# Optimization experiments

Hardware: AMD Instinct MI355X
Metric: run time of the kernel (lower is better)

## Reference

```python
import jax, jax.numpy as jnp
import numpy as np

LATENT, HID, STYLE, D, B = 16, 512, 64, 8, 16384


def _lin(key, fan_in, fan_out):
    kw, kb = jax.random.split(key)
    s = 1.0 / np.sqrt(fan_in)
    return (jax.random.uniform(kw, (fan_in, fan_out), jnp.float32, -s, s),
            jax.random.uniform(kb, (fan_out,), jnp.float32, -s, s))


def setup_inputs() -> dict:
    key = jax.random.key(0)
    ks = jax.random.split(key, 12)
    x = jax.random.normal(ks[0], (B, LATENT), jnp.float32)
    y = jax.random.randint(ks[1], (B,), 0, D)
    # shared MLP: latent->512, 512->512 x3, each followed by ReLU
    W0, b0 = _lin(ks[2], LATENT, HID)
    W1, b1 = _lin(ks[3], HID, HID)
    W2, b2 = _lin(ks[4], HID, HID)
    W3, b3 = _lin(ks[5], HID, HID)
    # unshared per-domain 4-layer MLPs, stacked along domain axis d
    def _stack(k, fi, fo):
        Ws, bs = [], []
        for kk in jax.random.split(k, D):
            w, b = _lin(kk, fi, fo)
            Ws.append(w); bs.append(b)
        return jnp.stack(Ws), jnp.stack(bs)
    U0, c0 = _stack(ks[6], HID, HID)
    U1, c1 = _stack(ks[7], HID, HID)
    U2, c2 = _stack(ks[8], HID, HID)
    U3, c3 = _stack(ks[9], HID, STYLE)
    return {"x": x, "y": y,
            "W0": W0, "b0": b0, "W1": W1, "b1": b1,
            "W2": W2, "b2": b2, "W3": W3, "b3": b3,
            "U0": U0, "c0": c0, "U1": U1, "c1": c1,
            "U2": U2, "c2": c2, "U3": U3, "c3": c3}


def reference(x, y, W0, b0, W1, b1, W2, b2, W3, b3,
              U0, c0, U1, c1, U2, c2, U3, c3):
    # shared trunk
    h = jax.nn.relu(x @ W0 + b0)
    h = jax.nn.relu(h @ W1 + b1)
    h = jax.nn.relu(h @ W2 + b2)
    h = jax.nn.relu(h @ W3 + b3)            # [B, HID]
    # run all D expert MLPs batched, then select per-sample by domain y
    g = jax.nn.relu(jnp.einsum('bi,dio->dbo', h, U0) + c0[:, None, :])
    g = jax.nn.relu(jnp.einsum('dbi,dio->dbo', g, U1) + c1[:, None, :])
    g = jax.nn.relu(jnp.einsum('dbi,dio->dbo', g, U2) + c2[:, None, :])
    g = jnp.einsum('dbi,dio->dbo', g, U3) + c3[:, None, :]   # [D, B, STYLE]
    out = g[y, jnp.arange(g.shape[1])]       # [B, STYLE]
    return out
```

## Files before the change

### kernel.cpp

```cpp
#include <hip/hip_runtime.h>

typedef _Float16 f16;
typedef _Float16 f16x4 __attribute__((ext_vector_type(4)));
typedef _Float16 f16x8 __attribute__((ext_vector_type(8)));
typedef float f32x4 __attribute__((ext_vector_type(4)));

#define B_TOT 16384
#define LAT_  16
#define STY_  64
#define ND_   8

#define ROWS 64
#define NTHR 1024
#define NBLK 256

#define RSTR 40
#define SLAB (64 * RSTR)
#define ACT_LDS (16 * SLAB)

__global__ void prep_k(const float* W0, f16* Wt0, const float* W1, f16* Wt1,
                       const float* W2, f16* Wt2, const float* W3, f16* Wt3,
                       const float* U0, f16* U0t, const float* U1, f16* U1t,
                       const float* U2, f16* U2t, const float* U3, f16* U3t) {
  int z = blockIdx.z;
  const float* src; f16* dst; int Kin, Nin, Kpad, NR;
  if (z == 0)      { src = W0; dst = Wt0; Kin = 16;  Nin = 512; Kpad = 32;  NR = 512; }
  else if (z == 1) { src = W1; dst = Wt1; Kin = 512; Nin = 512; Kpad = 512; NR = 512; }
  else if (z == 2) { src = W2; dst = Wt2; Kin = 512; Nin = 512; Kpad = 512; NR = 512; }
  else if (z == 3) { src = W3; dst = Wt3; Kin = 512; Nin = 512; Kpad = 512; NR = 512; }
  else if (z < 12) { int d = z - 4;  src = U0 + (long)d * 262144; dst = U0t + (long)d * 262144; Kin = 512; Nin = 512; Kpad = 512; NR = 512; }
  else if (z < 20) { int d = z - 12; src = U1 + (long)d * 262144; dst = U1t + (long)d * 262144; Kin = 512; Nin = 512; Kpad = 512; NR = 512; }
  else if (z < 28) { int d = z - 20; src = U2 + (long)d * 262144; dst = U2t + (long)d * 262144; Kin = 512; Nin = 512; Kpad = 512; NR = 512; }
  else             { int d = z - 28; src = U3 + (long)d * 32768;  dst = U3t + (long)d * 32768;  Kin = 512; Nin = 64;  Kpad = 512; NR = 64; }

  __shared__ float tile[32][33];
  int k0 = blockIdx.y * 32, n0 = blockIdx.x * 32;
  int tx = threadIdx.x, ty = threadIdx.y;
  #pragma unroll
  for (int i = 0; i < 32; i += 8) {
    int k = k0 + ty + i, n = n0 + tx;
    tile[ty + i][tx] = (k < Kin && n < Nin) ? src[(long)k * Nin + n] : 0.f;
  }
  __syncthreads();
  #pragma unroll
  for (int i = 0; i < 32; i += 8) {
    int n = n0 + ty + i, k = k0 + tx;
    if (n < NR && k < Kpad)
      dst[(long)(((k >> 5) * NR + n) << 5) | (k & 31)] = (f16)tile[tx][ty + i];
  }
}

#define NT_BUCKET 1024
#define RPT 16

__global__ __launch_bounds__(NT_BUCKET) void bucket_k(const int* __restrict__ y,
                                                      int* __restrict__ offsets,
                                                      int* __restrict__ perm) {
  __shared__ int hist[ND_][NT_BUCKET];
  __shared__ int totals[ND_];
  __shared__ int bases[ND_ + 1];
  int t = threadIdx.x;
  int base = t * RPT;

  #pragma unroll
  for (int d = 0; d < ND_; d++) hist[d][t] = 0;
  int yv[RPT];
  #pragma unroll
  for (int i = 0; i < RPT; i++) {
    yv[i] = y[base + i];
    hist[yv[i]][t]++;
  }
  __syncthreads();

  int wave = t >> 6, lane = t & 63;
  if (wave < ND_) {
    int d = wave;
    int carry = 0;
    for (int c = 0; c < NT_BUCKET; c += 64) {
      int v = hist[d][c + lane];
      int s = v;
      #pragma unroll
      for (int off = 1; off < 64; off <<= 1) {
        int u = __shfl_up(s, off, 64);
        if (lane >= off) s += u;
      }
      hist[d][c + lane] = carry + s - v;
      carry += __shfl(s, 63, 64);
    }
    if (lane == 0) totals[d] = carry;
  }
  __syncthreads();

  if (t == 0) {
    int s = 0;
    #pragma unroll
    for (int d = 0; d < ND_; d++) { bases[d] = s; offsets[d] = s; s += totals[d]; }
    bases[ND_] = s; offsets[ND_] = s;
  }
  __syncthreads();

  #pragma unroll
  for (int i = 0; i < RPT; i++) {
    int d = yv[i];
    int pos = bases[d] + hist[d][t];
    hist[d][t]++;
    perm[pos] = base + i;
  }
}

#define MFMA_(b, a, c) __builtin_amdgcn_mfma_f32_16x16x32_f16((b), (a), (c), 0, 0, 0)

template<int KT, bool FINAL>
__device__ __forceinline__ void do_layer(
    const f16* __restrict__ Wk, const float* __restrict__ bias,
    f16* __restrict__ act, int rlo, int rhi,
    const int* __restrict__ perm, int slot0, float* __restrict__ out, int t) {
  const int lane = t & 63, wid = t >> 6;
  const int lr = lane & 15, lg = lane >> 4;
  char* actb = (char*)act;

  __syncthreads();

  if (!FINAL) {
    const int wn = wid * 32;
    const f16* wp0 = Wk + ((wn + lr) * 32 + lg * 8);
    const f16* wp1 = Wk + ((wn + 16 + lr) * 32 + lg * 8);
    const char* ab[4];
    #pragma unroll
    for (int m = 0; m < 4; m++)
      ab[m] = actb + (m * 16 + lr) * 80 + lg * 16;

    f32x4 acc[4][2];
    #pragma unroll
    for (int m = 0; m < 4; m++) {
      acc[m][0] = f32x4{0.f, 0.f, 0.f, 0.f};
      acc[m][1] = f32x4{0.f, 0.f, 0.f, 0.f};
    }

    f16x8 a0[4], a1[4], b00, b01, b10, b11;
    b00 = *(const f16x8*)wp0;
    b01 = *(const f16x8*)wp1;
    #pragma unroll
    for (int m = 0; m < 4; m++) a0[m] = *(const f16x8*)(ab[m]);

    if constexpr (KT == 1) {
      #pragma unroll
      for (int m = 0; m < 4; m++) {
        acc[m][0] = MFMA_(b00, a0[m], acc[m][0]);
        acc[m][1] = MFMA_(b01, a0[m], acc[m][1]);
      }
    } else {
      #pragma unroll
      for (int kt2 = 0; kt2 < KT / 2; kt2++) {
        const int k1 = 2 * kt2 + 1, k2 = 2 * kt2 + 2;
        b10 = *(const f16x8*)(wp0 + k1 * 16384);
        b11 = *(const f16x8*)(wp1 + k1 * 16384);
        #pragma unroll
        for (int m = 0; m < 4; m++) a1[m] = *(const f16x8*)(ab[m] + k1 * 5120);
        #pragma unroll
        for (int m = 0; m < 4; m++) {
          acc[m][0] = MFMA_(b00, a0[m], acc[m][0]);
          acc[m][1] = MFMA_(b01, a0[m], acc[m][1]);
        }
        if (kt2 < KT / 2 - 1) {
          b00 = *(const f16x8*)(wp0 + k2 * 16384);
          b01 = *(const f16x8*)(wp1 + k2 * 16384);
          #pragma unroll
          for (int m = 0; m < 4; m++) a0[m] = *(const f16x8*)(ab[m] + k2 * 5120);
        }
        #pragma unroll
        for (int m = 0; m < 4; m++) {
          acc[m][0] = MFMA_(b10, a1[m], acc[m][0]);
          acc[m][1] = MFMA_(b11, a1[m], acc[m][1]);
        }
      }
    }

    __syncthreads();

    #pragma unroll
    for (int m = 0; m < 4; m++) {
      int r = m * 16 + lr;
      bool ok = (r >= rlo) && (r < rhi);
      #pragma unroll
      for (int n = 0; n < 2; n++) {
        int cl = n * 16 + lg * 4;
        f32x4 bb = *(const f32x4*)(bias + wn + cl);
        f16x4 h;
        #pragma unroll
        for (int j = 0; j < 4; j++)
          h[j] = (f16)fmaxf(acc[m][n][j] + bb[j], 0.f);
        if (ok)
          *(f16x4*)(actb + wid * 5120 + r * 80 + cl * 2) = h;
      }
    }
  } else {
    const int mf = wid >> 2, nf = wid & 3;
    const f16* wp = Wk + ((nf * 16 + lr) * 32 + lg * 8);
    const char* abf = actb + (mf * 16 + lr) * 80 + lg * 16;
    f32x4 a = f32x4{0.f, 0.f, 0.f, 0.f};
    #pragma unroll
    for (int kt = 0; kt < 16; kt++) {
      f16x8 bf = *(const f16x8*)(wp + kt * 2048);
      f16x8 af = *(const f16x8*)(abf + kt * 5120);
      a = MFMA_(bf, af, a);
    }
    int r = mf * 16 + lr;
    if (r >= rlo && r < rhi) {
      int orig = perm[slot0 + r];
      int cn0 = nf * 16 + lg * 4;
      f32x4 bb = *(const f32x4*)(bias + cn0);
      f32x4 v;
      #pragma unroll
      for (int j = 0; j < 4; j++) v[j] = a[j] + bb[j];
      *(f32x4*)(out + (long)orig * STY_ + cn0) = v;
    }
  }
}

__global__ __launch_bounds__(NTHR, 4) void fused_k(
    const float* __restrict__ x,
    const f16* __restrict__ Wt0, const float* __restrict__ b0,
    const f16* __restrict__ Wt1, const float* __restrict__ b1,
    const f16* __restrict__ Wt2, const float* __restrict__ b2,
    const f16* __restrict__ Wt3, const float* __restrict__ b3,
    const f16* __restrict__ U0t, const float* __restrict__ c0,
    const f16* __restrict__ U1t, const float* __restrict__ c1,
    const f16* __restrict__ U2t, const float* __restrict__ c2,
    const f16* __restrict__ U3t, const float* __restrict__ c3,
    const int* __restrict__ offs, const int* __restrict__ perm,
    float* __restrict__ out) {
  __shared__ f16 act[ACT_LDS];

  int t = threadIdx.x;
  int wg = (blockIdx.x & 7) * (NBLK / 8) + (blockIdx.x >> 3);
  int slot0 = wg * ROWS;

  char* actb = (char*)act;
  #pragma unroll
  for (int i = 0; i < 2; i++) {
    int e = i * NTHR + t;
    int r = e >> 5, c = e & 31;
    int orig = perm[slot0 + r];
    f16 v = (c < LAT_) ? (f16)x[orig * LAT_ + c] : (f16)0.f;
    *(f16*)(actb + r * 80 + c * 2) = v;
  }

  int d0 = 0, d1 = 0;
  #pragma unroll
  for (int d = 1; d < ND_; d++) {
    d0 += (slot0 >= offs[d]);
    d1 += (slot0 + ROWS - 1 >= offs[d]);
  }

  do_layer<1,  false>(Wt0, b0, act, 0, ROWS, perm, slot0, out, t);
  do_layer<16, false>(Wt1, b1, act, 0, ROWS, perm, slot0, out, t);
  do_layer<16, false>(Wt2, b2, act, 0, ROWS, perm, slot0, out, t);
  do_layer<16, false>(Wt3, b3, act, 0, ROWS, perm, slot0, out, t);

  #pragma unroll 1
  for (int d = d0; d <= d1; d++) {
    int rlo = (d == d0) ? 0 : (offs[d] - slot0);
    int rhi = (d == d1) ? ROWS : (offs[d + 1] - slot0);
    do_layer<16, false>(U0t + (long)d * 262144, c0 + d * 512,
                        act, rlo, rhi, perm, slot0, out, t);
  }
  #pragma unroll 1
  for (int d = d0; d <= d1; d++) {
    int rlo = (d == d0) ? 0 : (offs[d] - slot0);
    int rhi = (d == d1) ? ROWS : (offs[d + 1] - slot0);
    do_layer<16, false>(U1t + (long)d * 262144, c1 + d * 512,
                        act, rlo, rhi, perm, slot0, out, t);
  }
  #pragma unroll 1
  for (int d = d0; d <= d1; d++) {
    int rlo = (d == d0) ? 0 : (offs[d] - slot0);
    int rhi = (d == d1) ? ROWS : (offs[d + 1] - slot0);
    do_layer<16, false>(U2t + (long)d * 262144, c2 + d * 512,
                        act, rlo, rhi, perm, slot0, out, t);
  }
  #pragma unroll 1
  for (int d = d0; d <= d1; d++) {
    int rlo = (d == d0) ? 0 : (offs[d] - slot0);
    int rhi = (d == d1) ? ROWS : (offs[d + 1] - slot0);
    do_layer<16, true>(U3t + (long)d * 32768, c3 + d * 64,
                       act, rlo, rhi, perm, slot0, out, t);
  }
}


extern "C" void kernel_launch(void* const* d_in, const int* in_sizes, int n_in,
                              void* d_out, int out_size, void* d_ws, size_t ws_size,
                              hipStream_t stream) {
  const float* x  = (const float*)d_in[0];
  const int*   y  = (const int*)  d_in[1];
  const float* W0 = (const float*)d_in[2];
  const float* b0 = (const float*)d_in[3];
  const float* W1 = (const float*)d_in[4];
  const float* b1 = (const float*)d_in[5];
  const float* W2 = (const float*)d_in[6];
  const float* b2 = (const float*)d_in[7];
  const float* W3 = (const float*)d_in[8];
  const float* b3 = (const float*)d_in[9];
  const float* U0 = (const float*)d_in[10];
  const float* c0 = (const float*)d_in[11];
  const float* U1 = (const float*)d_in[12];
  const float* c1 = (const float*)d_in[13];
  const float* U2 = (const float*)d_in[14];
  const float* c2 = (const float*)d_in[15];
  const float* U3 = (const float*)d_in[16];
  const float* c3 = (const float*)d_in[17];
  float* out = (float*)d_out;

  char* p = (char*)d_ws;
  auto alloc = [&](size_t bytes) -> char* {
    char* r = p; p += (bytes + 255) & ~(size_t)255; return r;
  };
  f16* Wt0 = (f16*)alloc((size_t)512 * 32 * 2);
  f16* Wt1 = (f16*)alloc((size_t)512 * 512 * 2);
  f16* Wt2 = (f16*)alloc((size_t)512 * 512 * 2);
  f16* Wt3 = (f16*)alloc((size_t)512 * 512 * 2);
  f16* U0t = (f16*)alloc((size_t)ND_ * 512 * 512 * 2);
  f16* U1t = (f16*)alloc((size_t)ND_ * 512 * 512 * 2);
  f16* U2t = (f16*)alloc((size_t)ND_ * 512 * 512 * 2);
  f16* U3t = (f16*)alloc((size_t)ND_ * 16 * 64 * 32 * 2);
  int* offsets = (int*)alloc((ND_ + 1) * 4);
  int* perm    = (int*)alloc((size_t)B_TOT * 4);

  prep_k<<<dim3(16, 16, 36), dim3(32, 8), 0, stream>>>(W0, Wt0, W1, Wt1, W2, Wt2, W3, Wt3,
                                                       U0, U0t, U1, U1t, U2, U2t, U3, U3t);
  bucket_k<<<1, NT_BUCKET, 0, stream>>>(y, offsets, perm);
  fused_k<<<NBLK, NTHR, 0, stream>>>(x, Wt0, b0, Wt1, b1, Wt2, b2, Wt3, b3,
                                     U0t, c0, U1t, c1, U2t, c2, U3t, c3,
                                     offsets, perm, out);
}
```

Measured before the change: 114.0 us.

## Halve block threads and widen per-wave tile to 64 columns with deeper prefetch

Cuts the block from 16 to 8 waves. Each wave now computes a 64x64 output tile (4x4 MFMA fragments) instead of 64x32, so every activation fragment read from LDS is reused across twice as many columns. The K loop is rewritten as a single software pipeline: weights are prefetched two steps ahead in a triple buffer and activations one step ahead. The final layer and input staging are remapped to the new wave count. The cost is roughly double the accumulator registers (launch bounds lowered to 2 blocks per CU) and fewer waves available to hide latency.

```diff
diff --git a/kernel.cpp b/kernel.cpp
--- a/kernel.cpp
+++ b/kernel.cpp
@@ -11,7 +11,7 @@
 #define ND_   8
 
 #define ROWS 64
-#define NTHR 1024
+#define NTHR 512
 #define NBLK 256
 
 #define RSTR 40
@@ -122,58 +122,49 @@
   __syncthreads();
 
   if (!FINAL) {
-    const int wn = wid * 32;
-    const f16* wp0 = Wk + ((wn + lr) * 32 + lg * 8);
-    const f16* wp1 = Wk + ((wn + 16 + lr) * 32 + lg * 8);
+    const int wn = wid * 64;
+    const f16* wp[4];
+    #pragma unroll
+    for (int n = 0; n < 4; n++)
+      wp[n] = Wk + ((wn + n * 16 + lr) * 32 + lg * 8);
     const char* ab[4];
     #pragma unroll
     for (int m = 0; m < 4; m++)
       ab[m] = actb + (m * 16 + lr) * 80 + lg * 16;
 
-    f32x4 acc[4][2];
-    #pragma unroll
-    for (int m = 0; m < 4; m++) {
-      acc[m][0] = f32x4{0.f, 0.f, 0.f, 0.f};
-      acc[m][1] = f32x4{0.f, 0.f, 0.f, 0.f};
-    }
-
-    f16x8 a0[4], a1[4], b00, b01, b10, b11;
-    b00 = *(const f16x8*)wp0;
-    b01 = *(const f16x8*)wp1;
-    #pragma unroll
-    for (int m = 0; m < 4; m++) a0[m] = *(const f16x8*)(ab[m]);
-
-    if constexpr (KT == 1) {
-      #pragma unroll
-      for (int m = 0; m < 4; m++) {
-        acc[m][0] = MFMA_(b00, a0[m], acc[m][0]);
-        acc[m][1] = MFMA_(b01, a0[m], acc[m][1]);
+    f32x4 acc[4][4];
+    #pragma unroll
+    for (int m = 0; m < 4; m++)
+      #pragma unroll
+      for (int n = 0; n < 4; n++) acc[m][n] = f32x4{0.f, 0.f, 0.f, 0.f};
+
+    f16x8 bf[3][4], af[2][4];
+    #pragma unroll
+    for (int n = 0; n < 4; n++) bf[0][n] = *(const f16x8*)(wp[n]);
+    if constexpr (KT > 1) {
+      #pragma unroll
+      for (int n = 0; n < 4; n++) bf[1][n] = *(const f16x8*)(wp[n] + 16384);
+    }
+    #pragma unroll
+    for (int m = 0; m < 4; m++) af[0][m] = *(const f16x8*)(ab[m]);
+
+    #pragma unroll
+    for (int kt = 0; kt < KT; kt++) {
+      if (kt + 2 < KT) {
+        #pragma unroll
+        for (int n = 0; n < 4; n++)
+          bf[(kt + 2) % 3][n] = *(const f16x8*)(wp[n] + (kt + 2) * 16384);
       }
-    } else {
-      #pragma unroll
-      for (int kt2 = 0; kt2 < KT / 2; kt2++) {
-        const int k1 = 2 * kt2 + 1, k2 = 2 * kt2 + 2;
-        b10 = *(const f16x8*)(wp0 + k1 * 16384);
-        b11 = *(const f16x8*)(wp1 + k1 * 16384);
+      if (kt + 1 < KT) {
         #pragma unroll
-        for (int m = 0; m < 4; m++) a1[m] = *(const f16x8*)(ab[m] + k1 * 5120);
+        for (int m = 0; m < 4; m++)
+          af[(kt + 1) % 2][m] = *(const f16x8*)(ab[m] + (kt + 1) * 5120);
+      }
+      #pragma unroll
+      for (int m = 0; m < 4; m++)
         #pragma unroll
-        for (int m = 0; m < 4; m++) {
-          acc[m][0] = MFMA_(b00, a0[m], acc[m][0]);
-          acc[m][1] = MFMA_(b01, a0[m], acc[m][1]);
-        }
-        if (kt2 < KT / 2 - 1) {
-          b00 = *(const f16x8*)(wp0 + k2 * 16384);
-          b01 = *(const f16x8*)(wp1 + k2 * 16384);
-          #pragma unroll
-          for (int m = 0; m < 4; m++) a0[m] = *(const f16x8*)(ab[m] + k2 * 5120);
-        }
-        #pragma unroll
-        for (int m = 0; m < 4; m++) {
-          acc[m][0] = MFMA_(b10, a1[m], acc[m][0]);
-          acc[m][1] = MFMA_(b11, a1[m], acc[m][1]);
-        }
-      }
+        for (int n = 0; n < 4; n++)
+          acc[m][n] = MFMA_(bf[kt % 3][n], af[kt % 2][m], acc[m][n]);
     }
 
     __syncthreads();
@@ -183,42 +174,47 @@
       int r = m * 16 + lr;
       bool ok = (r >= rlo) && (r < rhi);
       #pragma unroll
-      for (int n = 0; n < 2; n++) {
-        int cl = n * 16 + lg * 4;
-        f32x4 bb = *(const f32x4*)(bias + wn + cl);
+      for (int n = 0; n < 4; n++) {
+        int cn0 = wn + n * 16 + lg * 4;
+        f32x4 bb = *(const f32x4*)(bias + cn0);
         f16x4 h;
         #pragma unroll
         for (int j = 0; j < 4; j++)
           h[j] = (f16)fmaxf(acc[m][n][j] + bb[j], 0.f);
+        int slab = 2 * wid + (n >> 1);
+        int cl = (n & 1) * 16 + lg * 4;
         if (ok)
-          *(f16x4*)(actb + wid * 5120 + r * 80 + cl * 2) = h;
+          *(f16x4*)(actb + slab * 5120 + r * 80 + cl * 2) = h;
       }
     }
   } else {
-    const int mf = wid >> 2, nf = wid & 3;
-    const f16* wp = Wk + ((nf * 16 + lr) * 32 + lg * 8);
+    const int mf = wid & 3, nfb = wid >> 2;
+    const f16* wp0 = Wk + ((nfb * 32 + lr) * 32 + lg * 8);
+    const f16* wp1 = Wk + ((nfb * 32 + 16 + lr) * 32 + lg * 8);
     const char* abf = actb + (mf * 16 + lr) * 80 + lg * 16;
-    f32x4 a = f32x4{0.f, 0.f, 0.f, 0.f};
+    f32x4 a0 = f32x4{0.f, 0.f, 0.f, 0.f}, a1 = a0;
     #pragma unroll
     for (int kt = 0; kt < 16; kt++) {
-      f16x8 bf = *(const f16x8*)(wp + kt * 2048);
       f16x8 af = *(const f16x8*)(abf + kt * 5120);
-      a = MFMA_(bf, af, a);
+      a0 = MFMA_(*(const f16x8*)(wp0 + kt * 2048), af, a0);
+      a1 = MFMA_(*(const f16x8*)(wp1 + kt * 2048), af, a1);
     }
     int r = mf * 16 + lr;
     if (r >= rlo && r < rhi) {
       int orig = perm[slot0 + r];
-      int cn0 = nf * 16 + lg * 4;
-      f32x4 bb = *(const f32x4*)(bias + cn0);
-      f32x4 v;
-      #pragma unroll
-      for (int j = 0; j < 4; j++) v[j] = a[j] + bb[j];
-      *(f32x4*)(out + (long)orig * STY_ + cn0) = v;
-    }
-  }
-}
-
-__global__ __launch_bounds__(NTHR, 4) void fused_k(
+      int cn0 = nfb * 32 + lg * 4;
+      f32x4 bb0 = *(const f32x4*)(bias + cn0);
+      f32x4 bb1 = *(const f32x4*)(bias + cn0 + 16);
+      f32x4 v0, v1;
+      #pragma unroll
+      for (int j = 0; j < 4; j++) { v0[j] = a0[j] + bb0[j]; v1[j] = a1[j] + bb1[j]; }
+      *(f32x4*)(out + (long)orig * STY_ + cn0) = v0;
+      *(f32x4*)(out + (long)orig * STY_ + cn0 + 16) = v1;
+    }
+  }
+}
+
+__global__ __launch_bounds__(NTHR, 2) void fused_k(
     const float* __restrict__ x,
     const f16* __restrict__ Wt0, const float* __restrict__ b0,
     const f16* __restrict__ Wt1, const float* __restrict__ b1,
@@ -238,7 +234,7 @@
 
   char* actb = (char*)act;
   #pragma unroll
-  for (int i = 0; i < 2; i++) {
+  for (int i = 0; i < 4; i++) {
     int e = i * NTHR + t;
     int r = e >> 5, c = e & 31;
     int orig = perm[slot0 + r];
```

Result: slower. 124.2 us (+8.9%).
